# Kernel tuning notes

Measured on AMD Instinct MI355X. Metric: run time of the kernel, lower is better.

Reference implementation:

```python
import jax, jax.numpy as jnp
import numpy as np
from jax import lax

T, B, HW, HID, NA = 128, 64, 52, 512, 15  # rollout len, num_envs, image size, lstm hidden, n_actions


def setup_inputs() -> dict:
    key = jax.random.key(0)
    ks = jax.random.split(key, 20)
    BT = T * B
    x = jax.random.uniform(ks[0], (BT, HW, HW, 3), dtype=jnp.float32) * 255.0
    done = jax.random.randint(ks[1], (BT,), 0, 2).astype(jnp.float32)
    h0 = jax.random.normal(ks[2], (B, HID), dtype=jnp.float32) * 0.1
    c0 = jax.random.normal(ks[3], (B, HID), dtype=jnp.float32) * 0.1
    action = jax.random.randint(ks[4], (BT,), 0, NA, dtype=jnp.int32)
    n = lambda k, s, sc: jax.random.normal(k, s, dtype=jnp.float32) * sc
    return {
        "x": x, "done": done, "h0": h0, "c0": c0, "action": action,
        "conv_w1": n(ks[5], (32, 3, 8, 8), 0.05), "conv_b1": jnp.zeros((32,), jnp.float32),
        "conv_w2": n(ks[6], (64, 32, 4, 4), 0.05), "conv_b2": jnp.zeros((64,), jnp.float32),
        "conv_w3": n(ks[7], (64, 64, 3, 3), 0.05), "conv_b3": jnp.zeros((64,), jnp.float32),
        "fc_w": n(ks[8], (576, HID), 0.05), "fc_b": jnp.zeros((HID,), jnp.float32),
        "w_ih": n(ks[9], (4 * HID, HID), 0.04), "w_hh": n(ks[10], (4 * HID, HID), 0.04),
        "b_lstm": jnp.zeros((4 * HID,), jnp.float32),
        "actor_w": n(ks[11], (HID, NA), 0.01), "actor_b": jnp.zeros((NA,), jnp.float32),
        "critic_w": n(ks[12], (HID, 1), 0.05), "critic_b": jnp.zeros((1,), jnp.float32),
    }


def _conv(x, w, b, stride):
    y = lax.conv_general_dilated(x, w, (stride, stride), "VALID",
                                 dimension_numbers=("NCHW", "OIHW", "NCHW"))
    return y + b[None, :, None, None]


def _forward(x, done, h0, c0, conv_w1, conv_b1, conv_w2, conv_b2, conv_w3, conv_b3,
             fc_w, fc_b, w_ih, w_hh, b_lstm, actor_w, actor_b, critic_w, critic_b, action):
    # CNN encoder (input arrives NHWC like the torch caller, permute to NCHW)
    z = jnp.transpose(x, (0, 3, 1, 2)) / 255.0
    z = jax.nn.relu(_conv(z, conv_w1, conv_b1, 4))   # [BT,32,12,12]
    z = jax.nn.relu(_conv(z, conv_w2, conv_b2, 2))   # [BT,64,5,5]
    z = jax.nn.relu(_conv(z, conv_w3, conv_b3, 1))   # [BT,64,3,3]
    z = z.reshape(z.shape[0], -1)                    # [BT,576]
    hidden = jax.nn.relu(z @ fc_w + fc_b)            # [BT,512]

    seq = hidden.reshape(T, B, HID)
    dseq = done.reshape(T, B)

    def step(carry, inp):
        h, c = carry
        xt, dt = inp
        m = (1.0 - dt)[:, None]                       # done-mask resets state
        h, c = h * m, c * m
        gates = xt @ w_ih.T + h @ w_hh.T + b_lstm     # [B,4H], gate order i,f,g,o
        i, f, g, o = jnp.split(gates, 4, axis=-1)
        i, f, o = jax.nn.sigmoid(i), jax.nn.sigmoid(f), jax.nn.sigmoid(o)
        c = f * c + i * jnp.tanh(g)
        h = o * jnp.tanh(c)
        return (h, c), h

    (hT, cT), hs = lax.scan(step, (h0, c0), (seq, dseq))
    feats = hs.reshape(T * B, HID)

    logits = feats @ actor_w + actor_b               # [BT,NA]
    logp = jax.nn.log_softmax(logits)
    lp_a = jnp.take_along_axis(logp, action[:, None], axis=1)[:, 0]
    entropy = -jnp.sum(jnp.exp(logp) * logp, axis=-1)
    value = feats @ critic_w + critic_b              # [BT,1]
    return lp_a, entropy, value, hT, cT


def reference(x, done, h0, c0, conv_w1, conv_b1, conv_w2, conv_b2, conv_w3, conv_b3,
              fc_w, fc_b, w_ih, w_hh, b_lstm, actor_w, actor_b, critic_w, critic_b, action):
    return _forward(x, done, h0, c0, conv_w1, conv_b1, conv_w2, conv_b2, conv_w3, conv_b3,
                    fc_w, fc_b, w_ih, w_hh, b_lstm, actor_w, actor_b, critic_w, critic_b, action)
```

## Files before the change

kernel.cpp:

```cpp
#include <hip/hip_runtime.h>
#include <hip/hip_bf16.h>
#include <math.h>

typedef unsigned short u16;
typedef __attribute__((ext_vector_type(8))) short bf16x8;
typedef __attribute__((ext_vector_type(4))) float f32x4;

__device__ inline u16 f2b(float f) {
  __hip_bfloat16 h = __float2bfloat16(f);
  return *(u16*)&h;
}

__global__ void __launch_bounds__(256) prep_k(
    const float* __restrict__ w1, const float* __restrict__ w2,
    const float* __restrict__ w3, const float* __restrict__ fcw,
    const float* __restrict__ whh, const float* __restrict__ done,
    const float* __restrict__ h0, const float* __restrict__ c0,
    u16* __restrict__ w1bh, u16* __restrict__ w2bh, u16* __restrict__ w3bh,
    u16* __restrict__ fcwT, float* __restrict__ whhT,
    float* __restrict__ hT0, float* __restrict__ cbuf) {
  int i = blockIdx.x * 256 + threadIdx.x;
  if (i < 8192) {
    int c = i >> 8, k = i & 255;
    int ky = k >> 5, rem = k & 31;
    float v = 0.f;
    if (rem < 24) {
      int kx = rem / 3, ch = rem - kx * 3;
      v = w1[((c * 3 + ch) * 8 + ky) * 8 + kx] * (1.0f / 255.0f);
    }
    w1bh[i] = f2b(v);
    return;
  }
  i -= 8192;
  if (i < 32768) {
    int c = i >> 9, k = i & 511;
    int ci = k & 31, kyx = k >> 5;
    int ky = kyx >> 2, kx = kyx & 3;
    w2bh[i] = f2b(w2[c * 512 + ci * 16 + ky * 4 + kx]);
    return;
  }
  i -= 32768;
  if (i < 36864) {
    int c = i / 576, k = i - c * 576;
    int ci = k & 63, kyx = k >> 6;
    int ky = kyx / 3, kx = kyx - ky * 3;
    w3bh[i] = f2b(w3[((c * 64 + ci) * 3 + ky) * 3 + kx]);
    return;
  }
  i -= 36864;
  if (i < 294912) {
    int o = i / 576, r = i - o * 576;
    int c = r & 63, yx = r >> 6;
    fcwT[i] = f2b(fcw[(c * 9 + yx) * 512 + o]);
    return;
  }
  i -= 294912;
  if (i < 1048576) {
    int j = i & 2047, k = i >> 11;
    whhT[i] = whh[j * 512 + k];
    return;
  }
  i -= 1048576;
  if (i < 32768) {
    int b = i & 63;
    int k = i >> 6;
    hT0[i] = h0[b * 512 + k] * (1.0f - done[b]);
    return;
  }
  i -= 32768;
  if (i < 32768) {
    int b = i >> 9;
    cbuf[i] = c0[i] * (1.0f - done[b]);
  }
}

__global__ void __launch_bounds__(256) conv1m_k(
    const float* __restrict__ x, const u16* __restrict__ w1bh,
    const float* __restrict__ b1, u16* __restrict__ a1h) {
  __shared__ u16 As[256 * 40];
  __shared__ u16 Bs[32 * 40];
  const int tid = threadIdx.x;
  const long bm = (long)blockIdx.x * 256;
  const int w = tid >> 6;
  const int lane = tid & 63;
  const int lr = lane & 15;
  const int lk = lane >> 4;
  const int wm = w * 64;
  const int r = (int)bm + tid;
  const int n = r / 144;
  const int p = r - n * 144;
  const int py = p / 12;
  const int px = p - py * 12;
  const long gbase = (long)n * 8112 + py * 624 + px * 12;
  f32x4 zero = {0.f, 0.f, 0.f, 0.f};
  f32x4 acc[4][2];
#pragma unroll
  for (int mi = 0; mi < 4; ++mi)
#pragma unroll
    for (int ni = 0; ni < 2; ++ni) acc[mi][ni] = zero;

  const ushort4 z4 = {0, 0, 0, 0};
  for (int ky = 0; ky < 8; ++ky) {
    const float* src = x + gbase + ky * 156;
    float4 v[6];
#pragma unroll
    for (int q = 0; q < 6; ++q) v[q] = *(const float4*)&src[q * 4];
    u16* dst = &As[tid * 40];
#pragma unroll
    for (int q = 0; q < 6; ++q) {
      ushort4 o;
      o.x = f2b(v[q].x); o.y = f2b(v[q].y);
      o.z = f2b(v[q].z); o.w = f2b(v[q].w);
      *(ushort4*)&dst[q * 4] = o;
    }
    *(ushort4*)&dst[24] = z4;
    *(ushort4*)&dst[28] = z4;
    if (tid < 128) {
      const int c = tid >> 2, q = tid & 3;
      *(uint4*)&Bs[c * 40 + q * 8] = *(const uint4*)&w1bh[c * 256 + ky * 32 + q * 8];
    }
    __syncthreads();
    bf16x8 af[4], bfr[2];
#pragma unroll
    for (int mi = 0; mi < 4; ++mi)
      af[mi] = *(const bf16x8*)&As[(wm + mi * 16 + lr) * 40 + lk * 8];
#pragma unroll
    for (int ni = 0; ni < 2; ++ni)
      bfr[ni] = *(const bf16x8*)&Bs[(ni * 16 + lr) * 40 + lk * 8];
#pragma unroll
    for (int mi = 0; mi < 4; ++mi)
#pragma unroll
      for (int ni = 0; ni < 2; ++ni)
        acc[mi][ni] = __builtin_amdgcn_mfma_f32_16x16x32_bf16(
            af[mi], bfr[ni], acc[mi][ni], 0, 0, 0);
    __syncthreads();
  }
#pragma unroll
  for (int ni = 0; ni < 2; ++ni) {
    float bv = b1[ni * 16 + lr];
#pragma unroll
    for (int mi = 0; mi < 4; ++mi) {
#pragma unroll
      for (int j = 0; j < 4; ++j) {
        long rg = bm + wm + mi * 16 + lk * 4 + j;
        float v = fmaxf(acc[mi][ni][j] + bv, 0.f);
        a1h[rg * 32 + ni * 16 + lr] = f2b(v);
      }
    }
  }
}

__global__ void __launch_bounds__(256) conv2m_k(
    const u16* __restrict__ a1h, const u16* __restrict__ w2bh,
    const float* __restrict__ b2, u16* __restrict__ a2h) {
  __shared__ u16 As[256 * 40];
  __shared__ u16 Bs[64 * 40];
  const int tid = threadIdx.x;
  const long bm = (long)blockIdx.x * 256;
  const int w = tid >> 6;
  const int lane = tid & 63;
  const int lr = lane & 15;
  const int lk = lane >> 4;
  const int wm = w * 64;
  const int r = (int)bm + tid;
  const int n = r / 25;
  const int p = r - n * 25;
  const int py = p / 5;
  const int px = p - py * 5;
  const int pbase = n * 4608 + (py * 24 + px * 2) * 32;
  f32x4 zero = {0.f, 0.f, 0.f, 0.f};
  f32x4 acc[4][4];
#pragma unroll
  for (int mi = 0; mi < 4; ++mi)
#pragma unroll
    for (int ni = 0; ni < 4; ++ni) acc[mi][ni] = zero;

  for (int ks = 0; ks < 16; ++ks) {
    const int koff = ((ks >> 2) * 12 + (ks & 3)) * 32;
#pragma unroll
    for (int q = 0; q < 4; ++q)
      *(uint4*)&As[tid * 40 + q * 8] = *(const uint4*)&a1h[pbase + koff + q * 8];
    {
      const int c = tid >> 2, q = tid & 3;
      *(uint4*)&Bs[c * 40 + q * 8] = *(const uint4*)&w2bh[c * 512 + ks * 32 + q * 8];
    }
    __syncthreads();
    bf16x8 af[4], bfr[4];
#pragma unroll
    for (int mi = 0; mi < 4; ++mi)
      af[mi] = *(const bf16x8*)&As[(wm + mi * 16 + lr) * 40 + lk * 8];
#pragma unroll
    for (int ni = 0; ni < 4; ++ni)
      bfr[ni] = *(const bf16x8*)&Bs[(ni * 16 + lr) * 40 + lk * 8];
#pragma unroll
    for (int mi = 0; mi < 4; ++mi)
#pragma unroll
      for (int ni = 0; ni < 4; ++ni)
        acc[mi][ni] = __builtin_amdgcn_mfma_f32_16x16x32_bf16(
            af[mi], bfr[ni], acc[mi][ni], 0, 0, 0);
    __syncthreads();
  }
#pragma unroll
  for (int ni = 0; ni < 4; ++ni) {
    float bv = b2[ni * 16 + lr];
#pragma unroll
    for (int mi = 0; mi < 4; ++mi) {
#pragma unroll
      for (int j = 0; j < 4; ++j) {
        long rg = bm + wm + mi * 16 + lk * 4 + j;
        float v = fmaxf(acc[mi][ni][j] + bv, 0.f);
        a2h[rg * 64 + ni * 16 + lr] = f2b(v);
      }
    }
  }
}

__global__ void __launch_bounds__(256) conv3m_k(
    const u16* __restrict__ a2h, const u16* __restrict__ w3bh,
    const float* __restrict__ b3, u16* __restrict__ a3h) {
  __shared__ u16 As[256 * 40];
  __shared__ u16 Bs[64 * 40];
  const int tid = threadIdx.x;
  const long bm = (long)blockIdx.x * 256;
  const int w = tid >> 6;
  const int lane = tid & 63;
  const int lr = lane & 15;
  const int lk = lane >> 4;
  const int wm = w * 64;
  const int r = (int)bm + tid;
  const int n = r / 9;
  const int p = r - n * 9;
  const int py = p / 3;
  const int px = p - py * 3;
  const int pbase = n * 1600 + (py * 5 + px) * 64;
  f32x4 zero = {0.f, 0.f, 0.f, 0.f};
  f32x4 acc[4][4];
#pragma unroll
  for (int mi = 0; mi < 4; ++mi)
#pragma unroll
    for (int ni = 0; ni < 4; ++ni) acc[mi][ni] = zero;

  for (int ks2 = 0; ks2 < 18; ++ks2) {
    const int tap = ks2 >> 1;
    const int ky = tap / 3, kx = tap - ky * 3;
    const int koff = (ky * 5 + kx) * 64 + (ks2 & 1) * 32;
#pragma unroll
    for (int q = 0; q < 4; ++q)
      *(uint4*)&As[tid * 40 + q * 8] = *(const uint4*)&a2h[pbase + koff + q * 8];
    {
      const int c = tid >> 2, q = tid & 3;
      *(uint4*)&Bs[c * 40 + q * 8] = *(const uint4*)&w3bh[c * 576 + ks2 * 32 + q * 8];
    }
    __syncthreads();
    bf16x8 af[4], bfr[4];
#pragma unroll
    for (int mi = 0; mi < 4; ++mi)
      af[mi] = *(const bf16x8*)&As[(wm + mi * 16 + lr) * 40 + lk * 8];
#pragma unroll
    for (int ni = 0; ni < 4; ++ni)
      bfr[ni] = *(const bf16x8*)&Bs[(ni * 16 + lr) * 40 + lk * 8];
#pragma unroll
    for (int mi = 0; mi < 4; ++mi)
#pragma unroll
      for (int ni = 0; ni < 4; ++ni)
        acc[mi][ni] = __builtin_amdgcn_mfma_f32_16x16x32_bf16(
            af[mi], bfr[ni], acc[mi][ni], 0, 0, 0);
    __syncthreads();
  }
#pragma unroll
  for (int ni = 0; ni < 4; ++ni) {
    float bv = b3[ni * 16 + lr];
#pragma unroll
    for (int mi = 0; mi < 4; ++mi) {
#pragma unroll
      for (int j = 0; j < 4; ++j) {
        long rg = bm + wm + mi * 16 + lk * 4 + j;
        float v = fmaxf(acc[mi][ni][j] + bv, 0.f);
        a3h[rg * 64 + ni * 16 + lr] = f2b(v);
      }
    }
  }
}

__global__ void __launch_bounds__(256) cast_k(
    const float4* __restrict__ wihv, ushort4* __restrict__ wihh) {
  int i = blockIdx.x * 256 + threadIdx.x;
  if (i < 262144) {
    float4 v = wihv[i];
    ushort4 o;
    o.x = f2b(v.x); o.y = f2b(v.y); o.z = f2b(v.z); o.w = f2b(v.w);
    wihh[i] = o;
  }
}

__global__ void __launch_bounds__(256) mgemm_k(
    const u16* __restrict__ A, const u16* __restrict__ B,
    const float* __restrict__ bias, float* __restrict__ Cf,
    u16* __restrict__ Ch, const int K, const int N,
    const int RELU, const int OUTBF16) {
  __shared__ u16 As[128 * 40];
  __shared__ u16 Bs[128 * 40];
  const int tid = threadIdx.x;
  const long bm = (long)blockIdx.x * 128;
  const long bn = (long)blockIdx.y * 128;
  const int w = tid >> 6;
  const int lane = tid & 63;
  const int lr = lane & 15;
  const int lk = lane >> 4;
  const int wm = (w >> 1) * 64, wn = (w & 1) * 64;
  f32x4 zero = {0.f, 0.f, 0.f, 0.f};
  f32x4 acc[4][4];
#pragma unroll
  for (int mi = 0; mi < 4; ++mi)
#pragma unroll
    for (int ni = 0; ni < 4; ++ni) acc[mi][ni] = zero;

  for (int k0 = 0; k0 < K; k0 += 32) {
#pragma unroll
    for (int q = 0; q < 2; ++q) {
      int idx = tid * 2 + q;
      int row = idx >> 2, kq = (idx & 3) * 8;
      *(uint4*)&As[row * 40 + kq] = *(const uint4*)&A[(bm + row) * K + k0 + kq];
      *(uint4*)&Bs[row * 40 + kq] = *(const uint4*)&B[(bn + row) * K + k0 + kq];
    }
    __syncthreads();
    bf16x8 af[4], bfr[4];
#pragma unroll
    for (int mi = 0; mi < 4; ++mi)
      af[mi] = *(const bf16x8*)&As[(wm + mi * 16 + lr) * 40 + lk * 8];
#pragma unroll
    for (int ni = 0; ni < 4; ++ni)
      bfr[ni] = *(const bf16x8*)&Bs[(wn + ni * 16 + lr) * 40 + lk * 8];
#pragma unroll
    for (int mi = 0; mi < 4; ++mi)
#pragma unroll
      for (int ni = 0; ni < 4; ++ni)
        acc[mi][ni] = __builtin_amdgcn_mfma_f32_16x16x32_bf16(
            af[mi], bfr[ni], acc[mi][ni], 0, 0, 0);
    __syncthreads();
  }
#pragma unroll
  for (int ni = 0; ni < 4; ++ni) {
    float bv = bias[bn + wn + ni * 16 + lr];
#pragma unroll
    for (int mi = 0; mi < 4; ++mi) {
#pragma unroll
      for (int j = 0; j < 4; ++j) {
        long rg = bm + wm + mi * 16 + lk * 4 + j;
        long cg = bn + wn + ni * 16 + lr;
        float v = acc[mi][ni][j] + bv;
        if (RELU) v = fmaxf(v, 0.f);
        if (OUTBF16) Ch[rg * N + cg] = f2b(v);
        else Cf[rg * N + cg] = v;
      }
    }
  }
}

__global__ void __launch_bounds__(256) lstm_step_k(
    const float* __restrict__ gx, const float* __restrict__ whhT,
    const float* __restrict__ done, float* __restrict__ hT2,
    float* __restrict__ cbuf, float* __restrict__ hseq,
    float* __restrict__ outh, float* __restrict__ outc, const int t) {
  __shared__ float red[256][37];
  const int tid = threadIdx.x;
  const int bid = blockIdx.x;
  const int uslice = (bid & 7) * 4 + (bid >> 6);
  const int bg = (bid >> 3) & 7;
  const int uu = tid & 15;
  const int kc = tid >> 4;
  const int u = uslice * 16 + uu;
  const int b0 = bg * 8;
  const int fbl = tid >> 4;

  const float* hTp = hT2 + (t & 1) * 32768;
  float a0[8] = {0.f}, a1_[8] = {0.f}, a2_[8] = {0.f}, a3_[8] = {0.f};
  const int kbeg = kc * 32;
#pragma unroll 4
  for (int kk = 0; kk < 32; ++kk) {
    int k = kbeg + kk;
    const float* wr = whhT + k * 2048;
    float w0 = wr[u];
    float w1 = wr[u + 512];
    float w2 = wr[u + 1024];
    float w3 = wr[u + 1536];
    float hv[8];
    *(float4*)&hv[0] = *(const float4*)&hTp[k * 64 + b0];
    *(float4*)&hv[4] = *(const float4*)&hTp[k * 64 + b0 + 4];
#pragma unroll
    for (int j = 0; j < 8; ++j) {
      a0[j] += w0 * hv[j]; a1_[j] += w1 * hv[j];
      a2_[j] += w2 * hv[j]; a3_[j] += w3 * hv[j];
    }
  }
#pragma unroll
  for (int j = 0; j < 8; ++j) {
    red[tid][j] = a0[j];       red[tid][8 + j] = a1_[j];
    red[tid][16 + j] = a2_[j]; red[tid][24 + j] = a3_[j];
  }
  __syncthreads();
  if (fbl < 8) {
    float s0 = 0.f, s1 = 0.f, s2 = 0.f, s3 = 0.f;
#pragma unroll
    for (int q = 0; q < 16; ++q) {
      const float* rp = red[q * 16 + uu];
      s0 += rp[fbl]; s1 += rp[8 + fbl]; s2 += rp[16 + fbl]; s3 += rp[24 + fbl];
    }
    const int b = b0 + fbl;
    const int ug = uslice * 16 + uu;
    const int row = t * 64 + b;
    const float* gxr = gx + (long)row * 2048;
    float pi = s0 + gxr[ug];
    float pf = s1 + gxr[512 + ug];
    float pg_ = s2 + gxr[1024 + ug];
    float po = s3 + gxr[1536 + ug];
    float ig = 1.f / (1.f + expf(-pi));
    float fg = 1.f / (1.f + expf(-pf));
    float og = 1.f / (1.f + expf(-po));
    float gg = tanhf(pg_);
    float cn = fg * cbuf[b * 512 + ug] + ig * gg;
    float hn = og * tanhf(cn);
    hseq[(long)row * 512 + ug] = hn;
    if (t == 127) {
      outh[b * 512 + ug] = hn;
      outc[b * 512 + ug] = cn;
    } else {
      float mn = 1.f - done[(t + 1) * 64 + b];
      cbuf[b * 512 + ug] = cn * mn;
      hT2[((t + 1) & 1) * 32768 + ug * 64 + b] = hn * mn;
    }
  }
}

__global__ void __launch_bounds__(256) heads_k(
    const float* __restrict__ hseq, const float* __restrict__ aw,
    const float* __restrict__ ab, const float* __restrict__ cw,
    const float* __restrict__ cb, const int* __restrict__ action,
    float* __restrict__ out) {
  const int lane = threadIdx.x & 63;
  const int wid = threadIdx.x >> 6;
  const int row = blockIdx.x * 4 + wid;
  const int j = lane & 15;
  const int kc = lane >> 4;
  const float* f = hseq + (long)row * 512;
  float acc = 0.f;
  if (j < 15) {
    for (int k = kc * 128; k < kc * 128 + 128; ++k) acc += f[k] * aw[k * 15 + j];
  } else {
    for (int k = kc * 128; k < kc * 128 + 128; ++k) acc += f[k] * cw[k];
  }
  acc += __shfl_xor(acc, 16);
  acc += __shfl_xor(acc, 32);
  float logit = (j < 15) ? acc + ab[j] : -1e30f;
  float m = logit;
#pragma unroll
  for (int off = 1; off < 16; off <<= 1) m = fmaxf(m, __shfl_xor(m, off));
  float p = (j < 15) ? expf(logit - m) : 0.f;
  float S = p;
#pragma unroll
  for (int off = 1; off < 16; off <<= 1) S += __shfl_xor(S, off);
  float logS = logf(S);
  float lp = logit - m - logS;
  float e = (j < 15) ? p * lp : 0.f;
  float es = e;
#pragma unroll
  for (int off = 1; off < 16; off <<= 1) es += __shfl_xor(es, off);
  float ent = -es / S;
  int a = action[row];
  float lpa = __shfl(lp, (lane & 48) | a);
  float val = __shfl(acc, (lane & 48) | 15) + cb[0];
  if (lane == 0) {
    out[row] = lpa;
    out[8192 + row] = ent;
    out[16384 + row] = val;
  }
}

extern "C" void kernel_launch(void* const* d_in, const int* in_sizes, int n_in,
                              void* d_out, int out_size, void* d_ws, size_t ws_size,
                              hipStream_t stream) {
  const float* x    = (const float*)d_in[0];
  const float* done = (const float*)d_in[1];
  const float* h0   = (const float*)d_in[2];
  const float* c0   = (const float*)d_in[3];
  const int*   act  = (const int*)d_in[4];
  const float* w1   = (const float*)d_in[5];
  const float* b1   = (const float*)d_in[6];
  const float* w2   = (const float*)d_in[7];
  const float* b2   = (const float*)d_in[8];
  const float* w3   = (const float*)d_in[9];
  const float* b3   = (const float*)d_in[10];
  const float* fcw  = (const float*)d_in[11];
  const float* fcb  = (const float*)d_in[12];
  const float* wih  = (const float*)d_in[13];
  const float* whh  = (const float*)d_in[14];
  const float* blst = (const float*)d_in[15];
  const float* aw   = (const float*)d_in[16];
  const float* ab   = (const float*)d_in[17];
  const float* cw   = (const float*)d_in[18];
  const float* cb   = (const float*)d_in[19];
  float* ws  = (float*)d_ws;
  float* out = (float*)d_out;

  u16*  a1h   = (u16*)ws;
  u16*  wihh  = (u16*)(ws + 4718592);
  float* hseq = ws + 8912896;
  u16*  a2h   = (u16*)(ws + 37748736);
  u16*  a3h   = (u16*)(ws + 44302336);
  u16*  hidh  = (u16*)(ws + 46661632);
  float* gxb  = ws + 50855936;
  u16*  w1bh  = (u16*)(ws + 67633152);
  u16*  w2bh  = (u16*)(ws + 67639296);
  u16*  w3bh  = (u16*)(ws + 67672064);
  u16*  fcwT  = (u16*)(ws + 67708928);
  float* whhT = ws + 68003840;
  float* hT2  = ws + 69052416;
  float* cbuf = ws + 69117952;

  hipLaunchKernelGGL(prep_k, dim3(5808), dim3(256), 0, stream,
                     w1, w2, w3, fcw, whh, done, h0, c0,
                     w1bh, w2bh, w3bh, fcwT, whhT, hT2, cbuf);
  hipLaunchKernelGGL(conv1m_k, dim3(4608), dim3(256), 0, stream, x, w1bh, b1, a1h);
  hipLaunchKernelGGL(conv2m_k, dim3(800), dim3(256), 0, stream, a1h, w2bh, b2, a2h);
  hipLaunchKernelGGL(conv3m_k, dim3(288), dim3(256), 0, stream, a2h, w3bh, b3, a3h);
  hipLaunchKernelGGL(cast_k, dim3(1024), dim3(256), 0, stream,
                     (const float4*)wih, (ushort4*)wihh);
  hipLaunchKernelGGL(mgemm_k, dim3(64, 4), dim3(256), 0, stream,
                     a3h, fcwT, fcb, (float*)nullptr, hidh, 576, 512, 1, 1);
  hipLaunchKernelGGL(mgemm_k, dim3(64, 16), dim3(256), 0, stream,
                     hidh, wihh, blst, gxb, (u16*)nullptr, 512, 2048, 0, 0);
  for (int t = 0; t < 128; ++t) {
    hipLaunchKernelGGL(lstm_step_k, dim3(256), dim3(256), 0, stream,
                       gxb, whhT, done, hT2, cbuf, hseq,
                       out + 24576, out + 57344, t);
  }
  hipLaunchKernelGGL(heads_k, dim3(2048), dim3(256), 0, stream,
                     hseq, aw, ab, cw, cb, act, out);
}
```

Before: 1.281 ms.

## Interleave LSTM recurrent weights by gate and halve batch per block

The recurrent weight matrix is re-laid out so the four gate weights for each hidden unit and k sit contiguously, letting each thread fetch them with one float4 load instead of four strided scalar loads. Each block now covers 4 batch rows instead of 8, so the per-step grid doubles to 512 blocks. Per-thread accumulators and the shared reduction buffer shrink to match. This is meant to raise parallelism in the latency-bound per-step kernel and cut register pressure, at the cost of reading the recurrent weights twice as often across blocks.

```diff
diff --git a/kernel.cpp b/kernel.cpp
--- a/kernel.cpp
+++ b/kernel.cpp
@@ -17,7 +17,7 @@
     const float* __restrict__ whh, const float* __restrict__ done,
     const float* __restrict__ h0, const float* __restrict__ c0,
     u16* __restrict__ w1bh, u16* __restrict__ w2bh, u16* __restrict__ w3bh,
-    u16* __restrict__ fcwT, float* __restrict__ whhT,
+    u16* __restrict__ fcwT, float* __restrict__ whhTi,
     float* __restrict__ hT0, float* __restrict__ cbuf) {
   int i = blockIdx.x * 256 + threadIdx.x;
   if (i < 8192) {
@@ -56,8 +56,11 @@
   }
   i -= 294912;
   if (i < 1048576) {
-    int j = i & 2047, k = i >> 11;
-    whhT[i] = whh[j * 512 + k];
+    int g = i & 3;
+    int rest = i >> 2;
+    int u = rest & 511;
+    int k = rest >> 9;
+    whhTi[i] = whh[((g * 512 + u) * 512) + k];
     return;
   }
   i -= 1048576;
@@ -358,56 +361,53 @@
 }
 
 __global__ void __launch_bounds__(256) lstm_step_k(
-    const float* __restrict__ gx, const float* __restrict__ whhT,
+    const float* __restrict__ gx, const float* __restrict__ whhTi,
     const float* __restrict__ done, float* __restrict__ hT2,
     float* __restrict__ cbuf, float* __restrict__ hseq,
     float* __restrict__ outh, float* __restrict__ outc, const int t) {
-  __shared__ float red[256][37];
+  __shared__ float red[256][17];
   const int tid = threadIdx.x;
   const int bid = blockIdx.x;
-  const int uslice = (bid & 7) * 4 + (bid >> 6);
-  const int bg = (bid >> 3) & 7;
+  const int uslice = (bid & 7) * 4 + (bid >> 7);
+  const int bg = (bid >> 3) & 15;
   const int uu = tid & 15;
   const int kc = tid >> 4;
   const int u = uslice * 16 + uu;
-  const int b0 = bg * 8;
-  const int fbl = tid >> 4;
+  const int b0 = bg * 4;
 
   const float* hTp = hT2 + (t & 1) * 32768;
-  float a0[8] = {0.f}, a1_[8] = {0.f}, a2_[8] = {0.f}, a3_[8] = {0.f};
+  float acc[4][4];
+#pragma unroll
+  for (int g = 0; g < 4; ++g)
+#pragma unroll
+    for (int j = 0; j < 4; ++j) acc[g][j] = 0.f;
   const int kbeg = kc * 32;
-#pragma unroll 4
+#pragma unroll 8
   for (int kk = 0; kk < 32; ++kk) {
-    int k = kbeg + kk;
-    const float* wr = whhT + k * 2048;
-    float w0 = wr[u];
-    float w1 = wr[u + 512];
-    float w2 = wr[u + 1024];
-    float w3 = wr[u + 1536];
-    float hv[8];
-    *(float4*)&hv[0] = *(const float4*)&hTp[k * 64 + b0];
-    *(float4*)&hv[4] = *(const float4*)&hTp[k * 64 + b0 + 4];
-#pragma unroll
-    for (int j = 0; j < 8; ++j) {
-      a0[j] += w0 * hv[j]; a1_[j] += w1 * hv[j];
-      a2_[j] += w2 * hv[j]; a3_[j] += w3 * hv[j];
-    }
-  }
-#pragma unroll
-  for (int j = 0; j < 8; ++j) {
-    red[tid][j] = a0[j];       red[tid][8 + j] = a1_[j];
-    red[tid][16 + j] = a2_[j]; red[tid][24 + j] = a3_[j];
-  }
+    const int k = kbeg + kk;
+    float4 w4 = *(const float4*)&whhTi[(k * 512 + u) * 4];
+    float4 hv = *(const float4*)&hTp[k * 64 + b0];
+    acc[0][0] += w4.x * hv.x; acc[0][1] += w4.x * hv.y; acc[0][2] += w4.x * hv.z; acc[0][3] += w4.x * hv.w;
+    acc[1][0] += w4.y * hv.x; acc[1][1] += w4.y * hv.y; acc[1][2] += w4.y * hv.z; acc[1][3] += w4.y * hv.w;
+    acc[2][0] += w4.z * hv.x; acc[2][1] += w4.z * hv.y; acc[2][2] += w4.z * hv.z; acc[2][3] += w4.z * hv.w;
+    acc[3][0] += w4.w * hv.x; acc[3][1] += w4.w * hv.y; acc[3][2] += w4.w * hv.z; acc[3][3] += w4.w * hv.w;
+  }
+#pragma unroll
+  for (int g = 0; g < 4; ++g)
+#pragma unroll
+    for (int j = 0; j < 4; ++j) red[tid][g * 4 + j] = acc[g][j];
   __syncthreads();
-  if (fbl < 8) {
+  if (tid < 64) {
+    const int fu = tid >> 2;
+    const int fb = tid & 3;
     float s0 = 0.f, s1 = 0.f, s2 = 0.f, s3 = 0.f;
 #pragma unroll
     for (int q = 0; q < 16; ++q) {
-      const float* rp = red[q * 16 + uu];
-      s0 += rp[fbl]; s1 += rp[8 + fbl]; s2 += rp[16 + fbl]; s3 += rp[24 + fbl];
-    }
-    const int b = b0 + fbl;
-    const int ug = uslice * 16 + uu;
+      const float* rp = red[q * 16 + fu];
+      s0 += rp[fb]; s1 += rp[4 + fb]; s2 += rp[8 + fb]; s3 += rp[12 + fb];
+    }
+    const int b = b0 + fb;
+    const int ug = uslice * 16 + fu;
     const int row = t * 64 + b;
     const float* gxr = gx + (long)row * 2048;
     float pi = s0 + gxr[ug];
@@ -513,13 +513,13 @@
   u16*  w2bh  = (u16*)(ws + 67639296);
   u16*  w3bh  = (u16*)(ws + 67672064);
   u16*  fcwT  = (u16*)(ws + 67708928);
-  float* whhT = ws + 68003840;
+  float* whhTi= ws + 68003840;
   float* hT2  = ws + 69052416;
   float* cbuf = ws + 69117952;
 
   hipLaunchKernelGGL(prep_k, dim3(5808), dim3(256), 0, stream,
                      w1, w2, w3, fcw, whh, done, h0, c0,
-                     w1bh, w2bh, w3bh, fcwT, whhT, hT2, cbuf);
+                     w1bh, w2bh, w3bh, fcwT, whhTi, hT2, cbuf);
   hipLaunchKernelGGL(conv1m_k, dim3(4608), dim3(256), 0, stream, x, w1bh, b1, a1h);
   hipLaunchKernelGGL(conv2m_k, dim3(800), dim3(256), 0, stream, a1h, w2bh, b2, a2h);
   hipLaunchKernelGGL(conv3m_k, dim3(288), dim3(256), 0, stream, a2h, w3bh, b3, a3h);
@@ -530,8 +530,8 @@
   hipLaunchKernelGGL(mgemm_k, dim3(64, 16), dim3(256), 0, stream,
                      hidh, wihh, blst, gxb, (u16*)nullptr, 512, 2048, 0, 0);
   for (int t = 0; t < 128; ++t) {
-    hipLaunchKernelGGL(lstm_step_k, dim3(256), dim3(256), 0, stream,
-                       gxb, whhT, done, hT2, cbuf, hseq,
+    hipLaunchKernelGGL(lstm_step_k, dim3(512), dim3(256), 0, stream,
+                       gxb, whhTi, done, hT2, cbuf, hseq,
                        out + 24576, out + 57344, t);
   }
   hipLaunchKernelGGL(heads_k, dim3(2048), dim3(256), 0, stream,
```

New measurement: 1.964 ms. +53.3%, slower.
